# Performance work log

Hardware: AMD Instinct MI355X
Metric: run time of the kernel (lower is better)

## Reference

```python
import jax, jax.numpy as jnp
import numpy as np

# norse LIFParameters defaults
DT = 1e-3
TAU_SYN_INV = 200.0   # 1/5e-3
TAU_MEM_INV = 100.0   # 1/1e-2
V_TH = 1.0            # v_leak = v_reset = 0
ALPHA = 100.0         # SuperSpike surrogate slope
SEQ_LEN = 10
F_MAX = 1000.0

@jax.custom_vjp
def superspike(x):
    # forward: heaviside(x > 0); backward: SuperSpike surrogate
    return (x > 0).astype(x.dtype)

def _ss_fwd(x):
    return (x > 0).astype(x.dtype), x

def _ss_bwd(x, g):
    return (g / (ALPHA * jnp.abs(x) + 1.0) ** 2,)

superspike.defvjp(_ss_fwd, _ss_bwd)

def lif_step(x, z, v, i, w_in, w_rec):
    # norse lif_step: decay, threshold, reset, then integrate synaptic current
    v_dec = v + DT * TAU_MEM_INV * (-v + i)      # v_leak = 0
    i_dec = i - DT * TAU_SYN_INV * i
    z_new = superspike(v_dec - V_TH)
    v_new = (1.0 - z_new) * v_dec                # v_reset = 0
    i_new = i_dec + x @ w_in.T + z @ w_rec.T     # uses OLD z for recurrence
    return z_new, v_new, i_new

def setup_inputs() -> dict:
    key = jax.random.key(0)
    k1, k2, k3, k4, k5 = jax.random.split(key, 5)
    B = 1048576
    return {
        "input_tensor": jax.random.uniform(k1, (B, 12), dtype=jnp.float32),
        "w_in0": jax.random.normal(k2, (6, 12), jnp.float32) * np.float32(np.sqrt(2.0 / 12)),
        "w_rec0": jax.random.normal(k3, (6, 6), jnp.float32) * np.float32(np.sqrt(2.0 / 6)),
        "w_in1": jax.random.normal(k4, (1, 6), jnp.float32) * np.float32(np.sqrt(2.0 / 6)),
        "w_rec1": jax.random.normal(k5, (1, 1), jnp.float32) * np.float32(np.sqrt(2.0)),
    }

def reference(input_tensor, w_in0, w_rec0, w_in1, w_rec1):
    B = input_tensor.shape[0]
    dtype = input_tensor.dtype
    # PoissonEncoder: spike = (rand < dt * f_max * x), shape [T, B, 12]
    u = jax.random.uniform(jax.random.key(42), (SEQ_LEN,) + input_tensor.shape, dtype=dtype)
    spike_ts = (u < DT * F_MAX * input_tensor).astype(dtype)

    def step(carry, x_t):
        z0, v0, i0, z1, v1, i1 = carry
        z0n, v0n, i0n = lif_step(x_t, z0, v0, i0, w_in0, w_rec0)
        z1n, v1n, i1n = lif_step(z0n, z1, v1, i1, w_in1, w_rec1)
        return (z0n, v0n, i0n, z1n, v1n, i1n), None

    zeros = lambda n: jnp.zeros((B, n), dtype)
    init = (zeros(6), zeros(6), zeros(6), zeros(1), zeros(1), zeros(1))
    (z0, v0, i0, z1, v1, i1), _ = jax.lax.scan(step, init, spike_ts)
    return z1  # final-timestep output spikes, [B, 1]
```

## Files before the change

kernel.cpp:

```cpp
#include <hip/hip_runtime.h>
#include <cstdint>


#define TFR(r) { x0 += x1; x1 = __builtin_amdgcn_alignbit(x1, x1, 32 - (r)); x1 ^= x0; }

__device__ __forceinline__ uint32_t tf_hash(uint32_t c) {
  uint32_t x0 = 0u;
  uint32_t x1 = c + 42u;
  TFR(13) TFR(15) TFR(26) TFR(6)
  x0 += 42u;          x1 += 0x1BD11BF1u;
  TFR(17) TFR(29) TFR(16) TFR(24)
  x0 += 0x1BD11BF0u;  x1 += 2u;
  TFR(13) TFR(15) TFR(26) TFR(6)
         x1 += 45u;
  TFR(17) TFR(29) TFR(16) TFR(24)
  x0 += 42u;          x1 += 0x1BD11BF4u;
  TFR(13) TFR(15) TFR(26) TFR(6)
  x0 += 0x1BD11BF0u;  x1 += 5u;
  return x0 ^ x1;
}

__global__ __launch_bounds__(256) void snn_kernel(
    const float* __restrict__ x_in, const float* __restrict__ w_in0,
    const float* __restrict__ w_rec0, const float* __restrict__ w_in1,
    const float* __restrict__ w_rec1, float* __restrict__ out, int B)
{
  int b = blockIdx.x * blockDim.x + threadIdx.x;
  if (b >= B) return;

  uint32_t T[12];
  {
    const float4* xv = reinterpret_cast<const float4*>(x_in + (size_t)b * 12);
    float4 q0 = xv[0], q1 = xv[1], q2 = xv[2];
    float x[12] = {q0.x,q0.y,q0.z,q0.w, q1.x,q1.y,q1.z,q1.w, q2.x,q2.y,q2.z,q2.w};
    #pragma unroll
    for (int j = 0; j < 12; ++j)
      T[j] = (uint32_t)__builtin_ceilf(x[j] * 8388608.0f);
  }

  float W0[6][12], R0[6][6], W1[6], R1;
  #pragma unroll
  for (int n = 0; n < 6; ++n) {
    #pragma unroll
    for (int j = 0; j < 12; ++j) W0[n][j] = w_in0[n * 12 + j];
  }
  #pragma unroll
  for (int n = 0; n < 6; ++n) {
    #pragma unroll
    for (int j = 0; j < 6; ++j) R0[n][j] = w_rec0[n * 6 + j];
  }
  #pragma unroll
  for (int j = 0; j < 6; ++j) W1[j] = w_in1[j];
  R1 = w_rec1[0];

  float v0[6], i0[6], z0[6];
  #pragma unroll
  for (int n = 0; n < 6; ++n) { v0[n] = 0.0f; i0[n] = 0.0f; z0[n] = 0.0f; }
  float v1 = 0.0f, i1 = 0.0f, z1 = 0.0f;

  const uint32_t t_stride = (uint32_t)B * 12u;
  uint32_t base = (uint32_t)b * 12u;

  #pragma unroll
  for (int t = 0; t < 10; ++t) {
    float sp[12];
    #pragma unroll
    for (int j = 0; j < 12; ++j) {
      uint32_t h = tf_hash(base + (uint32_t)j);
      sp[j] = ((h >> 9) < T[j]) ? 1.0f : 0.0f;
    }
    base += t_stride;

    float zn[6], vn[6], inew[6];
    #pragma unroll
    for (int n = 0; n < 6; ++n) {
      float vdec = __fadd_rn(v0[n], __fmul_rn(0.1f, __fsub_rn(i0[n], v0[n])));
      float idec = __fsub_rn(i0[n], __fmul_rn(0.2f, i0[n]));
      bool fire = (vdec > 1.0f);
      zn[n] = fire ? 1.0f : 0.0f;
      vn[n] = fire ? 0.0f : vdec;
      float d1 = 0.0f;
      #pragma unroll
      for (int j = 0; j < 12; ++j) d1 = __fmaf_rn(sp[j], W0[n][j], d1);
      float d2 = 0.0f;
      #pragma unroll
      for (int j = 0; j < 6; ++j) d2 = __fmaf_rn(z0[j], R0[n][j], d2);
      inew[n] = __fadd_rn(__fadd_rn(idec, d1), d2);
    }

    {
      float vdec = __fadd_rn(v1, __fmul_rn(0.1f, __fsub_rn(i1, v1)));
      float idec = __fsub_rn(i1, __fmul_rn(0.2f, i1));
      bool fire = (vdec > 1.0f);
      float z1n = fire ? 1.0f : 0.0f;
      float v1n = fire ? 0.0f : vdec;
      float d1 = 0.0f;
      #pragma unroll
      for (int j = 0; j < 6; ++j) d1 = __fmaf_rn(zn[j], W1[j], d1);
      float d2 = __fmaf_rn(z1, R1, 0.0f);
      float i1n = __fadd_rn(__fadd_rn(idec, d1), d2);
      z1 = z1n; v1 = v1n; i1 = i1n;
    }

    #pragma unroll
    for (int n = 0; n < 6; ++n) { z0[n] = zn[n]; v0[n] = vn[n]; i0[n] = inew[n]; }
  }

  out[b] = z1;
}

extern "C" void kernel_launch(void* const* d_in, const int* in_sizes, int n_in,
                              void* d_out, int out_size, void* d_ws, size_t ws_size,
                              hipStream_t stream) {
  const float* x      = (const float*)d_in[0];
  const float* w_in0  = (const float*)d_in[1];
  const float* w_rec0 = (const float*)d_in[2];
  const float* w_in1  = (const float*)d_in[3];
  const float* w_rec1 = (const float*)d_in[4];
  float* out = (float*)d_out;

  const int B = out_size;
  const int block = 256;
  const int grid = (B + block - 1) / block;
  snn_kernel<<<grid, block, 0, stream>>>(x, w_in0, w_rec0, w_in1, w_rec1, out, B);
}
```

Measured before the change: 280.9 us.

## Replace per-step dot products with precomputed spike-mask lookup tables and trim dead timesteps

Adds a small pre-kernel that tabulates every possible binary-spike dot product: 4096 input masks times 6 neurons, 64 recurrent masks, and 64 layer-1 masks. The main kernel then packs spikes into bitmasks and reads table entries instead of doing the FMAs. It also skips RNG for the last two timesteps and the state updates whose results cannot affect the final output. The aim is to cut ALU work, with gathers from a 128KB table in global memory (mostly cache-resident) as the cost. Summation order inside the table matches the original FMA chain, so results should stay bit-exact. The table path only runs when enough workspace is provided and otherwise falls back to the old kernel.

Result: faster. 266.7 us (-5.0%).

```diff
diff --git a/kernel.cpp b/kernel.cpp
--- a/kernel.cpp
+++ b/kernel.cpp
@@ -20,6 +20,133 @@
   return x0 ^ x1;
 }
 
+__global__ __launch_bounds__(256) void build_tables(
+    const float* __restrict__ w_in0, const float* __restrict__ w_rec0,
+    const float* __restrict__ w_in1, float* __restrict__ ws)
+{
+  int m = blockIdx.x * 256 + threadIdx.x;
+  float* tin = ws;
+  float* trc = ws + 32768;
+  float* tw1 = ws + 33280;
+  #pragma unroll
+  for (int n = 0; n < 6; ++n) {
+    float acc = 0.0f;
+    #pragma unroll
+    for (int j = 0; j < 12; ++j)
+      acc = __fmaf_rn(((m >> j) & 1) ? 1.0f : 0.0f, w_in0[n * 12 + j], acc);
+    tin[(m << 3) + n] = acc;
+  }
+  if (m < 64) {
+    #pragma unroll
+    for (int n = 0; n < 6; ++n) {
+      float acc = 0.0f;
+      #pragma unroll
+      for (int j = 0; j < 6; ++j)
+        acc = __fmaf_rn(((m >> j) & 1) ? 1.0f : 0.0f, w_rec0[n * 6 + j], acc);
+      trc[(m << 3) + n] = acc;
+    }
+    float acc = 0.0f;
+    #pragma unroll
+    for (int j = 0; j < 6; ++j)
+      acc = __fmaf_rn(((m >> j) & 1) ? 1.0f : 0.0f, w_in1[j], acc);
+    tw1[m] = acc;
+  }
+}
+
+__global__ __launch_bounds__(256) void snn_kernel_tbl(
+    const float* __restrict__ x_in, const float* __restrict__ w_rec1,
+    const float* __restrict__ tbl, float* __restrict__ out, int B)
+{
+  int b = blockIdx.x * blockDim.x + threadIdx.x;
+  if (b >= B) return;
+
+  const float* __restrict__ tin = tbl;
+  const float* __restrict__ trc = tbl + 32768;
+  const float* __restrict__ tw1 = tbl + 33280;
+
+  uint32_t TS[12];
+  {
+    const float4* xv = reinterpret_cast<const float4*>(x_in + (size_t)b * 12);
+    float4 q0 = xv[0], q1 = xv[1], q2 = xv[2];
+    float x[12] = {q0.x,q0.y,q0.z,q0.w, q1.x,q1.y,q1.z,q1.w, q2.x,q2.y,q2.z,q2.w};
+    #pragma unroll
+    for (int j = 0; j < 12; ++j)
+      TS[j] = ((uint32_t)__builtin_ceilf(x[j] * 8388608.0f)) << 9;
+  }
+
+  const uint32_t t_stride = (uint32_t)B * 12u;
+  uint32_t base = (uint32_t)b * 12u;
+  uint32_t msk[8];
+  #pragma unroll
+  for (int t = 0; t < 8; ++t) {
+    uint32_t m = 0;
+    #pragma unroll
+    for (int j = 0; j < 12; ++j) {
+      uint32_t h = tf_hash(base + (uint32_t)j);
+      m |= (h < TS[j]) ? (1u << j) : 0u;
+    }
+    msk[t] = m;
+    base += t_stride;
+  }
+
+  float4 dA[8]; float2 dB[8];
+  #pragma unroll
+  for (int t = 0; t < 8; ++t) {
+    const float* e = tin + (msk[t] << 3);
+    dA[t] = *reinterpret_cast<const float4*>(e);
+    dB[t] = *reinterpret_cast<const float2*>(e + 4);
+  }
+
+  float v0[6], i0[6];
+  #pragma unroll
+  for (int n = 0; n < 6; ++n) { v0[n] = 0.0f; i0[n] = 0.0f; }
+  uint32_t zm = 0;
+  float v1 = 0.0f, i1 = 0.0f, z1 = 0.0f;
+  const float R1 = w_rec1[0];
+
+  #pragma unroll
+  for (int t = 0; t < 10; ++t) {
+    uint32_t zmn = 0;
+    if (t < 9) {
+      float vdec[6];
+      #pragma unroll
+      for (int n = 0; n < 6; ++n) {
+        vdec[n] = __fadd_rn(v0[n], __fmul_rn(0.1f, __fsub_rn(i0[n], v0[n])));
+        zmn |= (vdec[n] > 1.0f) ? (1u << n) : 0u;
+      }
+      if (t < 8) {
+        const float* rc = trc + (zm << 3);
+        float4 r4 = *reinterpret_cast<const float4*>(rc);
+        float2 r2 = *reinterpret_cast<const float2*>(rc + 4);
+        float dR[6]  = {r4.x, r4.y, r4.z, r4.w, r2.x, r2.y};
+        float dAv[6] = {dA[t].x, dA[t].y, dA[t].z, dA[t].w, dB[t].x, dB[t].y};
+        #pragma unroll
+        for (int n = 0; n < 6; ++n) {
+          float idec = __fsub_rn(i0[n], __fmul_rn(0.2f, i0[n]));
+          v0[n] = (vdec[n] > 1.0f) ? 0.0f : vdec[n];
+          i0[n] = __fadd_rn(__fadd_rn(idec, dAv[n]), dR[n]);
+        }
+      }
+    }
+    {
+      float vdec = __fadd_rn(v1, __fmul_rn(0.1f, __fsub_rn(i1, v1)));
+      bool fire = (vdec > 1.0f);
+      float z1n = fire ? 1.0f : 0.0f;
+      if (t < 9) {
+        float idec = __fsub_rn(i1, __fmul_rn(0.2f, i1));
+        float d1 = tw1[zmn];
+        float d2 = __fmaf_rn(z1, R1, 0.0f);
+        i1 = __fadd_rn(__fadd_rn(idec, d1), d2);
+        v1 = fire ? 0.0f : vdec;
+      }
+      z1 = z1n;
+    }
+    zm = zmn;
+  }
+
+  out[b] = z1;
+}
+
 __global__ __launch_bounds__(256) void snn_kernel(
     const float* __restrict__ x_in, const float* __restrict__ w_in0,
     const float* __restrict__ w_rec0, const float* __restrict__ w_in1,
@@ -87,7 +214,6 @@
       for (int j = 0; j < 6; ++j) d2 = __fmaf_rn(z0[j], R0[n][j], d2);
       inew[n] = __fadd_rn(__fadd_rn(idec, d1), d2);
     }
-
     {
       float vdec = __fadd_rn(v1, __fmul_rn(0.1f, __fsub_rn(i1, v1)));
       float idec = __fsub_rn(i1, __fmul_rn(0.2f, i1));
@@ -101,7 +227,6 @@
       float i1n = __fadd_rn(__fadd_rn(idec, d1), d2);
       z1 = z1n; v1 = v1n; i1 = i1n;
     }
-
     #pragma unroll
     for (int n = 0; n < 6; ++n) { z0[n] = zn[n]; v0[n] = vn[n]; i0[n] = inew[n]; }
   }
@@ -122,5 +247,13 @@
   const int B = out_size;
   const int block = 256;
   const int grid = (B + block - 1) / block;
-  snn_kernel<<<grid, block, 0, stream>>>(x, w_in0, w_rec0, w_in1, w_rec1, out, B);
-}
+
+  const size_t WS_NEEDED = (size_t)(33280 + 64) * sizeof(float);
+  if (d_ws != nullptr && ws_size >= WS_NEEDED) {
+    float* tbl = (float*)d_ws;
+    build_tables<<<16, 256, 0, stream>>>(w_in0, w_rec0, w_in1, tbl);
+    snn_kernel_tbl<<<grid, block, 0, stream>>>(x, w_rec1, tbl, out, B);
+  } else {
+    snn_kernel<<<grid, block, 0, stream>>>(x, w_in0, w_rec0, w_in1, w_rec1, out, B);
+  }
+}
```
